# Kernel optimization log

Hardware: AMD Instinct MI355X
Metric: run time of the kernel (lower is better)

## Reference

```python
import jax, jax.numpy as jnp
import numpy as np

BATCH = 4
N_CTX = 1024
D_IN = 512
N_HEADS = 8
D_HEAD = 64
N_VARS = D_IN // D_HEAD  # ConstrainedRead default: n_vars = d_in // d_var = 8
TEMP = 1.0
ATTN_TEMP = float(np.sqrt(D_HEAD))  # attention_temp default = sqrt(d_head)


def setup_inputs() -> dict:
    key = jax.random.key(0)
    k1, k2, k3, k4, k5 = jax.random.split(key, 5)
    x = jax.random.uniform(k1, (BATCH, N_CTX, D_IN), dtype=jnp.float32)
    # causal tril mask, broadcast to batch (matches registered tril buffer usage)
    mask = jnp.broadcast_to(jnp.tril(jnp.ones((N_CTX, N_CTX), dtype=bool)), (BATCH, N_CTX, N_CTX))
    inv_sv = 1.0 / np.sqrt(N_VARS)
    W_K_W = jax.random.normal(k2, (N_HEADS, N_VARS), dtype=jnp.float32) * inv_sv
    W_Q_W = jax.random.normal(k3, (N_HEADS, N_VARS), dtype=jnp.float32) * inv_sv
    W_V_W = jax.random.normal(k4, (N_HEADS, N_VARS), dtype=jnp.float32) * inv_sv
    W_pred_W = jax.random.normal(k5, (N_HEADS, D_HEAD, D_HEAD), dtype=jnp.float32) / np.sqrt(D_HEAD)
    return {"x": x, "mask": mask, "W_K_W": W_K_W, "W_Q_W": W_Q_W, "W_V_W": W_V_W, "W_pred_W": W_pred_W}


def _constrained_read(W):
    # softmax over variables, then block-diagonal-style selector: (h, d_head, d_in)
    probs = jax.nn.softmax(W / TEMP, axis=-1)                 # (h, n_vars)
    eye = jnp.eye(D_HEAD, dtype=probs.dtype)                  # (c, c)
    rm = probs[:, :, None, None] * eye                        # (h, v, c, c)
    # einops 'a b c d -> a d (b c)'
    return jnp.transpose(rm, (0, 3, 1, 2)).reshape(N_HEADS, D_HEAD, D_IN)


def _fixed_bias_table():
    M = N_CTX  # table layout: [-2, linspace(0,-M,M-1)/M, linspace(-M,0,M)/M], shared over heads
    return jnp.concatenate([
        jnp.array([-2.0], dtype=jnp.float32),
        (jnp.linspace(0.0, -float(M), M - 1) / M).astype(jnp.float32),
        (jnp.linspace(-float(M), 0.0, M) / M).astype(jnp.float32),
    ])  # (2M,)


def reference(x, mask, W_K_W, W_Q_W, W_V_W, W_pred_W):
    WK = _constrained_read(W_K_W)
    WQm = _constrained_read(W_Q_W)
    WV = _constrained_read(W_V_W)
    # WPred: out[h,f,d] = sum_e W_Q[h,e,d] * softmax(W)[h,e,f]
    Wp = jax.nn.softmax(W_pred_W / TEMP, axis=-1)
    WQ = jnp.einsum('hed,hef->hfd', WQm, Wp)

    k = jnp.einsum('ihd,bpd->biph', WK, x)   # (b,h,p,dh)
    q = jnp.einsum('ihd,bpd->biph', WQ, x)
    v = jnp.einsum('ihd,bpd->biph', WV, x)

    pre = jnp.einsum('biph,biqh->biqp', k, q)            # (b,h,q,p)
    m = mask[:, None]                                    # (b,1,q,p)
    srow = jnp.where(m, pre, 0.0).sum(-1)                # (b,h,q)
    max_score = srow / (srow + 1e-10)
    pre = pre.at[:, :, :, 0].add(jax.nn.relu(1.0 - max_score))

    nq, nk = pre.shape[-2], pre.shape[-1]
    # relative position gather; %(2M) reproduces torch negative-index wraparound
    rel = (jnp.arange(nk)[None, :] - jnp.arange(nq)[:, None]) % (2 * N_CTX)
    bias = _fixed_bias_table()[rel]                      # (nq,nk), identical per head

    # one_hot_input=True: log(scores + 1e-20) + bias
    pos = jnp.log(pre + 1e-20) + bias[None, None]
    masked = jnp.where(m, pos, -1e30)
    attn = jax.nn.softmax(masked / ATTN_TEMP / TEMP, axis=-1)

    z = jnp.einsum('biph,biqp->biqh', v, attn)           # (b,h,q,dh)
    # einops 'b i q h -> b q (i h)'
    return jnp.transpose(z, (0, 2, 1, 3)).reshape(x.shape[0], nq, N_HEADS * D_HEAD)
```

## Files before the change

### kernel.cpp

```cpp
#include <hip/hip_runtime.h>
#include <math.h>

#define NCTX 1024
#define DIN 512
#define NH 8
#define DH 64

typedef float f32x16 __attribute__((ext_vector_type(16)));
typedef short bf16x8 __attribute__((ext_vector_type(8)));
typedef int i32x4 __attribute__((ext_vector_type(4)));

#define QF_OFF 0
#define KF_OFF (4u * 1024u * 1024u)
#define VF_OFF (8u * 1024u * 1024u)
#define V0_OFF (12u * 1024u * 1024u)

__device__ __forceinline__ bf16x8 asbf(i32x4 v) {
  union { i32x4 i; bf16x8 h; } u;
  u.i = v;
  return u.h;
}

__device__ __forceinline__ bf16x8 mk8(unsigned a, unsigned b, unsigned c,
                                      unsigned d) {
  union { unsigned u[4]; bf16x8 h; } x;
  x.u[0] = a; x.u[1] = b; x.u[2] = c; x.u[3] = d;
  return x.h;
}

__device__ __forceinline__ unsigned cvtpk(float lo, float hi_) {
  unsigned r;
  asm("v_cvt_pk_bf16_f32 %0, %1, %2" : "=v"(r) : "v"(lo), "v"(hi_));
  return r;
}

__device__ __forceinline__ void softmax8(const float* __restrict__ w,
                                         float* __restrict__ p) {
  float mx = w[0];
#pragma unroll
  for (int v = 1; v < 8; ++v) mx = fmaxf(mx, w[v]);
  float s = 0.f;
#pragma unroll
  for (int v = 0; v < 8; ++v) { p[v] = expf(w[v] - mx); s += p[v]; }
  const float inv = 1.f / s;
#pragma unroll
  for (int v = 0; v < 8; ++v) p[v] *= inv;
}

__global__ __launch_bounds__(256) void prep_kernel(
    const float* __restrict__ x, const float* __restrict__ WKw,
    const float* __restrict__ WQw, const float* __restrict__ WVw,
    const float* __restrict__ Wpred, short* __restrict__ Qf,
    short* __restrict__ Kf, short* __restrict__ Vf, float* __restrict__ V0f) {
  const int t = blockIdx.x, ih = blockIdx.y, b = blockIdx.z;
  const int bi = b * NH + ih;
  const int tid = threadIdx.x;

  __shared__ alignas(16) char smem[5 * 8192];
  char* const Ksb = smem;
  char* const Vtb = smem + 8192;
  char* const Q0b = smem + 16384;
  char* const WpT = smem + 24576;
  char* const Qsb = smem + 32768;

  {
    const int e = tid >> 2, sg = tid & 3;
    const float* wr = Wpred + (size_t)(ih * 64 + e) * 64 + sg * 16;
    float e16[16];
    float mx = -1e30f;
#pragma unroll
    for (int j = 0; j < 16; ++j) { e16[j] = wr[j]; mx = fmaxf(mx, e16[j]); }
    mx = fmaxf(mx, __shfl_xor(mx, 1, 4));
    mx = fmaxf(mx, __shfl_xor(mx, 2, 4));
    float s = 0.f;
#pragma unroll
    for (int j = 0; j < 16; ++j) { e16[j] = __expf(e16[j] - mx); s += e16[j]; }
    s += __shfl_xor(s, 1, 4);
    s += __shfl_xor(s, 2, 4);
    const float inv = 1.f / s;
#pragma unroll
    for (int j = 0; j < 16; ++j) {
      const int f = sg * 16 + j;
      const unsigned pz = cvtpk(e16[j] * inv, e16[j] * inv);
      *(unsigned short*)&WpT[f * 128 + ((2 * e) ^ ((f & 7) << 4))] =
          (unsigned short)pz;
    }
  }

  float pk[8], pq8[8], pv[8];
  {
    float w[8];
#pragma unroll
    for (int v = 0; v < 8; ++v) w[v] = WKw[ih * 8 + v];
    softmax8(w, pk);
#pragma unroll
    for (int v = 0; v < 8; ++v) w[v] = WQw[ih * 8 + v];
    softmax8(w, pq8);
#pragma unroll
    for (int v = 0; v < 8; ++v) w[v] = WVw[ih * 8 + v];
    softmax8(w, pv);
  }

  const int rg = tid >> 4, eg = tid & 15;
  const int r0 = rg * 4, e0 = eg * 4;
  float ka[4][4], qa[4][4], va[4][4];
#pragma unroll
  for (int i2 = 0; i2 < 4; ++i2)
#pragma unroll
    for (int j = 0; j < 4; ++j) { ka[i2][j] = 0.f; qa[i2][j] = 0.f; va[i2][j] = 0.f; }

  const float* xb = x + ((size_t)(b * NCTX + t * 64 + r0)) * DIN + e0;
#pragma unroll
  for (int v = 0; v < 8; ++v) {
#pragma unroll
    for (int i2 = 0; i2 < 4; ++i2) {
      const float4 xv = *(const float4*)(xb + (size_t)i2 * DIN + v * 64);
      ka[i2][0] = fmaf(pk[v], xv.x, ka[i2][0]);
      ka[i2][1] = fmaf(pk[v], xv.y, ka[i2][1]);
      ka[i2][2] = fmaf(pk[v], xv.z, ka[i2][2]);
      ka[i2][3] = fmaf(pk[v], xv.w, ka[i2][3]);
      qa[i2][0] = fmaf(pq8[v], xv.x, qa[i2][0]);
      qa[i2][1] = fmaf(pq8[v], xv.y, qa[i2][1]);
      qa[i2][2] = fmaf(pq8[v], xv.z, qa[i2][2]);
      qa[i2][3] = fmaf(pq8[v], xv.w, qa[i2][3]);
      va[i2][0] = fmaf(pv[v], xv.x, va[i2][0]);
      va[i2][1] = fmaf(pv[v], xv.y, va[i2][1]);
      va[i2][2] = fmaf(pv[v], xv.z, va[i2][2]);
      va[i2][3] = fmaf(pv[v], xv.w, va[i2][3]);
    }
  }

  if (t == 0 && rg == 0) {
    *(float4*)(V0f + bi * 64 + e0) =
        make_float4(va[0][0], va[0][1], va[0][2], va[0][3]);
  }

#pragma unroll
  for (int i2 = 0; i2 < 4; ++i2) {
    const int r = r0 + i2;
    const int boff = (2 * e0) ^ ((r & 7) << 4);
    *(uint2*)&Ksb[r * 128 + boff] =
        make_uint2(cvtpk(ka[i2][0], ka[i2][1]), cvtpk(ka[i2][2], ka[i2][3]));
    *(uint2*)&Q0b[r * 128 + boff] =
        make_uint2(cvtpk(qa[i2][0], qa[i2][1]), cvtpk(qa[i2][2], qa[i2][3]));
  }
#pragma unroll
  for (int j = 0; j < 4; ++j) {
    const int rr = e0 + j;
    *(uint2*)&Vtb[rr * 128 + ((2 * r0) ^ ((rr & 7) << 4))] =
        make_uint2(cvtpk(va[0][j], va[1][j]), cvtpk(va[2][j], va[3][j]));
  }
  __syncthreads();

  const int wv = tid >> 6;
  const int l = tid & 63;
  const int lm = l & 31;
  const int hi = l >> 5;

  const size_t fbase = (size_t)bi * 8192 + (size_t)t * 512;
#pragma unroll
  for (int c = 0; c < 2; ++c) {
    const int idx = c * 256 + tid;
    const int pq = idx >> 8, j = (idx >> 6) & 3, ll = idx & 63;
    const int krow = 32 * pq + (ll & 31);
    const i32x4 kfr = *(const i32x4*)
        &Ksb[krow * 128 + ((32 * j + 16 * (ll >> 5)) ^ ((krow & 7) << 4))];
    ((i32x4*)Kf)[fbase + idx] = kfr;
    const int vrow = 32 * (j & 1) + (ll & 31);
    const i32x4 vfr = *(const i32x4*)
        &Vtb[vrow * 128 +
             ((64 * pq + 32 * (j >> 1) + 16 * (ll >> 5)) ^ ((vrow & 7) << 4))];
    ((i32x4*)Vf)[fbase + idx] = vfr;
  }

  {
    const int qq = wv & 1, ff = wv >> 1;
    f32x16 dreg;
#pragma unroll
    for (int r = 0; r < 16; ++r) dreg[r] = 0.f;
    const int arow = 32 * qq + lm;
    const int brow = 32 * ff + lm;
#pragma unroll
    for (int kk = 0; kk < 4; ++kk) {
      const i32x4 af = *(const i32x4*)
          &Q0b[arow * 128 + ((32 * kk + 16 * hi) ^ ((arow & 7) << 4))];
      const i32x4 bfr = *(const i32x4*)
          &WpT[brow * 128 + ((32 * kk + 16 * hi) ^ ((brow & 7) << 4))];
      dreg = __builtin_amdgcn_mfma_f32_32x32x16_bf16(asbf(af), asbf(bfr),
                                                     dreg, 0, 0, 0);
    }
#pragma unroll
    for (int r = 0; r < 16; ++r) {
      const int q = 32 * qq + (r & 3) + 8 * (r >> 2) + 4 * hi;
      const int f = 32 * ff + lm;
      const unsigned pz = cvtpk(dreg[r], dreg[r]);
      *(unsigned short*)&Qsb[q * 128 + ((2 * f) ^ ((q & 7) << 4))] =
          (unsigned short)pz;
    }
  }
  __syncthreads();

#pragma unroll
  for (int c = 0; c < 2; ++c) {
    const int idx = c * 256 + tid;
    const int qq2 = idx >> 8, kk = (idx >> 6) & 3, ll = idx & 63;
    const int row = 32 * qq2 + (ll & 31);
    const i32x4 qfr = *(const i32x4*)
        &Qsb[row * 128 + ((32 * kk + 16 * (ll >> 5)) ^ ((row & 7) << 4))];
    ((i32x4*)Qf)[fbase + idx] = qfr;
  }
}

#if __has_builtin(__builtin_amdgcn_exp2f) && __has_builtin(__builtin_amdgcn_logf)
#define T_LOG(x) __builtin_amdgcn_logf(x)
#define T_EXP(x) __builtin_amdgcn_exp2f(x)
#define T_L 1.7628215e-4f
#define T_DIAG (-0.36067376f)
#else
#define T_LOG(x) __logf(x)
#define T_EXP(x) __expf(x)
#define T_L 1.2219941e-4f
#define T_DIAG (-0.25f)
#endif

__global__ __launch_bounds__(256) void attn_kernel(
    const short* __restrict__ Qf, const short* __restrict__ Kf,
    const short* __restrict__ Vf, float* __restrict__ out) {
  const int bx = blockIdx.x;
  const int a = bx >> 5;
  const int bi = bx & 31;
  const int qt = (a < 16) ? (15 - (a >> 1)) : ((a - 16) >> 1);
  const int qq = a & 1;
  const int b = bi >> 3, ih = bi & 7;
  const int tid = threadIdx.x;
  const int wv = tid >> 6;
  const int pq = wv & 1;
  const int ph = wv >> 1;
  const int l = tid & 63;
  const int hi = l >> 5;
  const int lm = l & 31;

  __shared__ float nbuf[3][32][64];
  __shared__ float rdn[4][32];
  __shared__ float rinv[32];

  const i32x4* Qp = (const i32x4*)Qf + (size_t)bi * 8192 + (size_t)qt * 512 +
                    qq * 256;
  const i32x4* Kp = (const i32x4*)Kf + (size_t)bi * 8192 + pq * 256;
  const i32x4* Vp = (const i32x4*)Vf + (size_t)bi * 8192 + pq * 256;

  bf16x8 qfr[4];
#pragma unroll
  for (int kk = 0; kk < 4; ++kk) qfr[kk] = asbf(Qp[kk * 64 + l]);

  f32x16 num0, num1, st;
#pragma unroll
  for (int r = 0; r < 16; ++r) { num0[r] = 0.f; num1[r] = 0.f; }
  float den = 0.f;
  const int qg = qt * 64 + 32 * qq + lm;
  const int qpb = qg - 32 * pq - 4 * hi;

  i32x4 kK[4], vV[4];

#define LOADK(PT)                                                       \
  do {                                                                  \
    const size_t o_ = (size_t)(PT) * 512;                               \
    _Pragma("unroll") for (int kk = 0; kk < 4; ++kk)                    \
        kK[kk] = Kp[o_ + kk * 64 + l];                                  \
  } while (0)

#define LOADV(PT)                                                       \
  do {                                                                  \
    const size_t o_ = (size_t)(PT) * 512;                               \
    _Pragma("unroll") for (int j = 0; j < 4; ++j)                       \
        vV[j] = Vp[o_ + j * 64 + l];                                    \
  } while (0)

#define QKSTEP()                                                             \
  do {                                                                       \
    _Pragma("unroll") for (int r = 0; r < 16; ++r) st[r] = 0.f;              \
    __builtin_amdgcn_s_setprio(1);                                           \
    _Pragma("unroll") for (int kk = 0; kk < 4; ++kk) st =                    \
        __builtin_amdgcn_mfma_f32_32x32x16_bf16(asbf(kK[kk]), qfr[kk],       \
                                                st, 0, 0, 0);                \
    __builtin_amdgcn_s_setprio(0);                                           \
  } while (0)

#define REPACK_PV()                                                          \
  do {                                                                       \
    asm("v_permlane32_swap_b32 %0, %1" : "+v"(P0), "+v"(P2));                \
    asm("v_permlane32_swap_b32 %0, %1" : "+v"(P1), "+v"(P3));                \
    asm("v_permlane32_swap_b32 %0, %1" : "+v"(P4), "+v"(P6));                \
    asm("v_permlane32_swap_b32 %0, %1" : "+v"(P5), "+v"(P7));                \
    const bf16x8 wf0 = mk8(P0, P1, P2, P3);                                  \
    const bf16x8 wf1 = mk8(P4, P5, P6, P7);                                  \
    __builtin_amdgcn_s_setprio(1);                                           \
    num0 = __builtin_amdgcn_mfma_f32_32x32x16_bf16(wf0, asbf(vV[0]),         \
                                                   num0, 0, 0, 0);           \
    num1 = __builtin_amdgcn_mfma_f32_32x32x16_bf16(wf0, asbf(vV[1]),         \
                                                   num1, 0, 0, 0);           \
    num0 = __builtin_amdgcn_mfma_f32_32x32x16_bf16(wf1, asbf(vV[2]),         \
                                                   num0, 0, 0, 0);           \
    num1 = __builtin_amdgcn_mfma_f32_32x32x16_bf16(wf1, asbf(vV[3]),         \
                                                   num1, 0, 0, 0);           \
    __builtin_amdgcn_s_setprio(0);                                           \
  } while (0)

  if (ph <= qt) {
    LOADK(ph);
    LOADV(ph);
    QKSTEP();
    if (ph + 2 <= qt) LOADK(ph + 2);

#pragma unroll 1
    for (int t = ph; t <= qt; t += 2) {
      const int D0 = qpb - 64 * t;
      const float B0 = (1.0f - (float)D0) * T_L;
      float d4_[4] = {0.f, 0.f, 0.f, 0.f};
      if (t == qt) {
#pragma unroll
        for (int r = 0; r < 16; ++r) {
          const int ro = (r & 3) + 8 * (r >> 2);
          const float pre = st[r];
          float b2 = B0 + (float)ro * T_L;
          b2 = (D0 == ro) ? T_DIAG : b2;
          b2 = (D0 < ro) ? -1e38f : b2;
          st[r] = T_EXP(fmaf(0.125f, T_LOG(pre + 1e-20f), b2));
          d4_[r & 3] += st[r];
        }
      } else {
#pragma unroll
        for (int r = 0; r < 16; ++r) {
          const int ro = (r & 3) + 8 * (r >> 2);
          const float b2 = B0 + (float)ro * T_L;
          st[r] = T_EXP(fmaf(0.125f, T_LOG(st[r] + 1e-20f), b2));
          d4_[r & 3] += st[r];
        }
      }
      den += (d4_[0] + d4_[1]) + (d4_[2] + d4_[3]);
      unsigned P0 = cvtpk(st[0], st[1]), P1 = cvtpk(st[2], st[3]);
      unsigned P2 = cvtpk(st[4], st[5]), P3 = cvtpk(st[6], st[7]);
      unsigned P4 = cvtpk(st[8], st[9]), P5 = cvtpk(st[10], st[11]);
      unsigned P6 = cvtpk(st[12], st[13]), P7 = cvtpk(st[14], st[15]);
      if (t + 2 <= qt) {
        QKSTEP();
        if (t + 4 <= qt) LOADK(t + 4);
      }
      REPACK_PV();
      if (t + 2 <= qt) LOADV(t + 2);
    }
  }

  const float den2 = den + __shfl_xor(den, 32, 64);
  if (hi == 0) rdn[wv][lm] = den2;
  if (wv != 0) {
#pragma unroll
    for (int r = 0; r < 16; ++r) {
      const int row = (r & 3) + 8 * (r >> 2) + 4 * hi;
      nbuf[wv - 1][row][lm] = num0[r];
      nbuf[wv - 1][row][32 + lm] = num1[r];
    }
  }
  __syncthreads();
  if (wv == 0 && hi == 0) {
    rinv[lm] = 1.f / (rdn[0][lm] + rdn[1][lm] + rdn[2][lm] + rdn[3][lm]);
  }
  __syncthreads();
  if (wv == 0) {
#pragma unroll
    for (int r = 0; r < 16; ++r) {
      const int row = (r & 3) + 8 * (r >> 2) + 4 * hi;
      const int qgq = qt * 64 + qq * 32 + row;
      const float iv = rinv[row];
      const float o0 = (num0[r] + nbuf[0][row][lm] + nbuf[1][row][lm] +
                        nbuf[2][row][lm]) * iv;
      const float o1 = (num1[r] + nbuf[0][row][32 + lm] +
                        nbuf[1][row][32 + lm] + nbuf[2][row][32 + lm]) * iv;
      float* op = out + ((size_t)b * NCTX + qgq) * DIN + ih * DH;
      op[lm] = o0;
      op[32 + lm] = o1;
    }
  }
#undef LOADK
#undef LOADV
#undef QKSTEP
#undef REPACK_PV
}

extern "C" void kernel_launch(void* const* d_in, const int* in_sizes, int n_in,
                              void* d_out, int out_size, void* d_ws,
                              size_t ws_size, hipStream_t stream) {
  const float* x = (const float*)d_in[0];
  const float* WKw = (const float*)d_in[2];
  const float* WQw = (const float*)d_in[3];
  const float* WVw = (const float*)d_in[4];
  const float* Wpred = (const float*)d_in[5];
  float* out = (float*)d_out;

  short* Qf = (short*)((char*)d_ws + QF_OFF);
  short* Kf = (short*)((char*)d_ws + KF_OFF);
  short* Vf = (short*)((char*)d_ws + VF_OFF);
  float* V0f = (float*)((char*)d_ws + V0_OFF);

  dim3 block(256);
  dim3 grid1(16, NH, 4);
  hipLaunchKernelGGL(prep_kernel, grid1, block, 0, stream, x, WKw, WQw, WVw,
                     Wpred, Qf, Kf, Vf, V0f);
  dim3 block2(256);
  dim3 grid2(1024);
  hipLaunchKernelGGL(attn_kernel, grid2, block2, 0, stream, Qf, Kf, Vf, out);
}
```

Baseline: 34.67 us.

## Share K/V tiles across two query halves via LDS double buffering

```diff
diff --git a/kernel.cpp b/kernel.cpp
--- a/kernel.cpp
+++ b/kernel.cpp
@@ -32,6 +32,12 @@
   unsigned r;
   asm("v_cvt_pk_bf16_f32 %0, %1, %2" : "=v"(r) : "v"(lo), "v"(hi_));
   return r;
+}
+
+__device__ __forceinline__ void gload_lds16(const i32x4* g, i32x4* lds) {
+  __builtin_amdgcn_global_load_lds(
+      (const __attribute__((address_space(1))) void*)g,
+      (__attribute__((address_space(3))) void*)lds, 16, 0, 0);
 }
 
 __device__ __forceinline__ void softmax8(const float* __restrict__ w,
@@ -229,25 +235,25 @@
   const int bx = blockIdx.x;
   const int a = bx >> 5;
   const int bi = bx & 31;
-  const int qt = (a < 16) ? (15 - (a >> 1)) : ((a - 16) >> 1);
-  const int qq = a & 1;
+  const int qt = (a < 8) ? (15 - a) : (a - 8);
   const int b = bi >> 3, ih = bi & 7;
   const int tid = threadIdx.x;
   const int wv = tid >> 6;
-  const int pq = wv & 1;
-  const int ph = wv >> 1;
   const int l = tid & 63;
   const int hi = l >> 5;
   const int lm = l & 31;
-
-  __shared__ float nbuf[3][32][64];
-  __shared__ float rdn[4][32];
-  __shared__ float rinv[32];
+  const int pq = wv & 1;
+  const int qq = wv >> 1;
+
+  __shared__ i32x4 kvbuf[2][1024];
+  __shared__ float num_l[2][32][64];
+  __shared__ float rdn[2][2][32];
+  __shared__ float rinv[2][32];
 
   const i32x4* Qp = (const i32x4*)Qf + (size_t)bi * 8192 + (size_t)qt * 512 +
                     qq * 256;
-  const i32x4* Kp = (const i32x4*)Kf + (size_t)bi * 8192 + pq * 256;
-  const i32x4* Vp = (const i32x4*)Vf + (size_t)bi * 8192 + pq * 256;
+  const i32x4* Kg = (const i32x4*)Kf + (size_t)bi * 8192;
+  const i32x4* Vg = (const i32x4*)Vf + (size_t)bi * 8192;
 
   bf16x8 qfr[4];
 #pragma unroll
@@ -260,131 +266,117 @@
   const int qg = qt * 64 + 32 * qq + lm;
   const int qpb = qg - 32 * pq - 4 * hi;
 
-  i32x4 kK[4], vV[4];
-
-#define LOADK(PT)                                                       \
-  do {                                                                  \
-    const size_t o_ = (size_t)(PT) * 512;                               \
-    _Pragma("unroll") for (int kk = 0; kk < 4; ++kk)                    \
-        kK[kk] = Kp[o_ + kk * 64 + l];                                  \
+#define STAGE(T, BUF)                                                        \
+  do {                                                                       \
+    const size_t o_ = (size_t)(T) * 512;                                     \
+    _Pragma("unroll") for (int c = 0; c < 4; ++c) {                          \
+      const int grp = wv * 4 + c;                                            \
+      const int idx = grp * 64 + l;                                          \
+      const i32x4* src = (grp < 8) ? (Kg + o_ + idx) : (Vg + o_ + idx - 512);\
+      gload_lds16(src, &kvbuf[BUF][grp * 64]);                               \
+    }                                                                        \
   } while (0)
 
-#define LOADV(PT)                                                       \
-  do {                                                                  \
-    const size_t o_ = (size_t)(PT) * 512;                               \
-    _Pragma("unroll") for (int j = 0; j < 4; ++j)                       \
-        vV[j] = Vp[o_ + j * 64 + l];                                    \
-  } while (0)
-
-#define QKSTEP()                                                             \
-  do {                                                                       \
-    _Pragma("unroll") for (int r = 0; r < 16; ++r) st[r] = 0.f;              \
-    __builtin_amdgcn_s_setprio(1);                                           \
-    _Pragma("unroll") for (int kk = 0; kk < 4; ++kk) st =                    \
-        __builtin_amdgcn_mfma_f32_32x32x16_bf16(asbf(kK[kk]), qfr[kk],       \
-                                                st, 0, 0, 0);                \
-    __builtin_amdgcn_s_setprio(0);                                           \
-  } while (0)
-
-#define REPACK_PV()                                                          \
-  do {                                                                       \
-    asm("v_permlane32_swap_b32 %0, %1" : "+v"(P0), "+v"(P2));                \
-    asm("v_permlane32_swap_b32 %0, %1" : "+v"(P1), "+v"(P3));                \
-    asm("v_permlane32_swap_b32 %0, %1" : "+v"(P4), "+v"(P6));                \
-    asm("v_permlane32_swap_b32 %0, %1" : "+v"(P5), "+v"(P7));                \
-    const bf16x8 wf0 = mk8(P0, P1, P2, P3);                                  \
-    const bf16x8 wf1 = mk8(P4, P5, P6, P7);                                  \
-    __builtin_amdgcn_s_setprio(1);                                           \
-    num0 = __builtin_amdgcn_mfma_f32_32x32x16_bf16(wf0, asbf(vV[0]),         \
-                                                   num0, 0, 0, 0);           \
-    num1 = __builtin_amdgcn_mfma_f32_32x32x16_bf16(wf0, asbf(vV[1]),         \
-                                                   num1, 0, 0, 0);           \
-    num0 = __builtin_amdgcn_mfma_f32_32x32x16_bf16(wf1, asbf(vV[2]),         \
-                                                   num0, 0, 0, 0);           \
-    num1 = __builtin_amdgcn_mfma_f32_32x32x16_bf16(wf1, asbf(vV[3]),         \
-                                                   num1, 0, 0, 0);           \
-    __builtin_amdgcn_s_setprio(0);                                           \
-  } while (0)
-
-  if (ph <= qt) {
-    LOADK(ph);
-    LOADV(ph);
-    QKSTEP();
-    if (ph + 2 <= qt) LOADK(ph + 2);
+  STAGE(0, 0);
+  __syncthreads();
 
 #pragma unroll 1
-    for (int t = ph; t <= qt; t += 2) {
-      const int D0 = qpb - 64 * t;
-      const float B0 = (1.0f - (float)D0) * T_L;
-      float d4_[4] = {0.f, 0.f, 0.f, 0.f};
-      if (t == qt) {
-#pragma unroll
-        for (int r = 0; r < 16; ++r) {
-          const int ro = (r & 3) + 8 * (r >> 2);
-          const float pre = st[r];
-          float b2 = B0 + (float)ro * T_L;
-          b2 = (D0 == ro) ? T_DIAG : b2;
-          b2 = (D0 < ro) ? -1e38f : b2;
-          st[r] = T_EXP(fmaf(0.125f, T_LOG(pre + 1e-20f), b2));
-          d4_[r & 3] += st[r];
-        }
-      } else {
-#pragma unroll
-        for (int r = 0; r < 16; ++r) {
-          const int ro = (r & 3) + 8 * (r >> 2);
-          const float b2 = B0 + (float)ro * T_L;
-          st[r] = T_EXP(fmaf(0.125f, T_LOG(st[r] + 1e-20f), b2));
-          d4_[r & 3] += st[r];
-        }
+  for (int t = 0; t <= qt; ++t) {
+    const int cur = t & 1;
+    if (t + 1 <= qt) STAGE(t + 1, cur ^ 1);
+
+    const i32x4 kK0 = kvbuf[cur][pq * 256 + l];
+    const i32x4 kK1 = kvbuf[cur][pq * 256 + 64 + l];
+    const i32x4 kK2 = kvbuf[cur][pq * 256 + 128 + l];
+    const i32x4 kK3 = kvbuf[cur][pq * 256 + 192 + l];
+#pragma unroll
+    for (int r = 0; r < 16; ++r) st[r] = 0.f;
+    __builtin_amdgcn_s_setprio(1);
+    st = __builtin_amdgcn_mfma_f32_32x32x16_bf16(asbf(kK0), qfr[0], st, 0, 0, 0);
+    st = __builtin_amdgcn_mfma_f32_32x32x16_bf16(asbf(kK1), qfr[1], st, 0, 0, 0);
+    st = __builtin_amdgcn_mfma_f32_32x32x16_bf16(asbf(kK2), qfr[2], st, 0, 0, 0);
+    st = __builtin_amdgcn_mfma_f32_32x32x16_bf16(asbf(kK3), qfr[3], st, 0, 0, 0);
+    __builtin_amdgcn_s_setprio(0);
+
+    const int D0 = qpb - 64 * t;
+    const float B0 = (1.0f - (float)D0) * T_L;
+    float d4_[4] = {0.f, 0.f, 0.f, 0.f};
+    if (t == qt) {
+#pragma unroll
+      for (int r = 0; r < 16; ++r) {
+        const int ro = (r & 3) + 8 * (r >> 2);
+        const float pre = st[r];
+        float b2 = B0 + (float)ro * T_L;
+        b2 = (D0 == ro) ? T_DIAG : b2;
+        b2 = (D0 < ro) ? -1e38f : b2;
+        st[r] = T_EXP(fmaf(0.125f, T_LOG(pre + 1e-20f), b2));
+        d4_[r & 3] += st[r];
       }
-      den += (d4_[0] + d4_[1]) + (d4_[2] + d4_[3]);
-      unsigned P0 = cvtpk(st[0], st[1]), P1 = cvtpk(st[2], st[3]);
-      unsigned P2 = cvtpk(st[4], st[5]), P3 = cvtpk(st[6], st[7]);
-      unsigned P4 = cvtpk(st[8], st[9]), P5 = cvtpk(st[10], st[11]);
-      unsigned P6 = cvtpk(st[12], st[13]), P7 = cvtpk(st[14], st[15]);
-      if (t + 2 <= qt) {
-        QKSTEP();
-        if (t + 4 <= qt) LOADK(t + 4);
+    } else {
+#pragma unroll
+      for (int r = 0; r < 16; ++r) {
+        const int ro = (r & 3) + 8 * (r >> 2);
+        const float b2 = B0 + (float)ro * T_L;
+        st[r] = T_EXP(fmaf(0.125f, T_LOG(st[r] + 1e-20f), b2));
+        d4_[r & 3] += st[r];
       }
-      REPACK_PV();
-      if (t + 2 <= qt) LOADV(t + 2);
-    }
+    }
+    den += (d4_[0] + d4_[1]) + (d4_[2] + d4_[3]);
+
+    unsigned P0 = cvtpk(st[0], st[1]), P1 = cvtpk(st[2], st[3]);
+    unsigned P2 = cvtpk(st[4], st[5]), P3 = cvtpk(st[6], st[7]);
+    unsigned P4 = cvtpk(st[8], st[9]), P5 = cvtpk(st[10], st[11]);
+    unsigned P6 = cvtpk(st[12], st[13]), P7 = cvtpk(st[14], st[15]);
+    asm("v_permlane32_swap_b32 %0, %1" : "+v"(P0), "+v"(P2));
+    asm("v_permlane32_swap_b32 %0, %1" : "+v"(P1), "+v"(P3));
+    asm("v_permlane32_swap_b32 %0, %1" : "+v"(P4), "+v"(P6));
+    asm("v_permlane32_swap_b32 %0, %1" : "+v"(P5), "+v"(P7));
+    const bf16x8 wf0 = mk8(P0, P1, P2, P3);
+    const bf16x8 wf1 = mk8(P4, P5, P6, P7);
+
+    const i32x4 vV0 = kvbuf[cur][512 + pq * 256 + l];
+    const i32x4 vV1 = kvbuf[cur][512 + pq * 256 + 64 + l];
+    const i32x4 vV2 = kvbuf[cur][512 + pq * 256 + 128 + l];
+    const i32x4 vV3 = kvbuf[cur][512 + pq * 256 + 192 + l];
+    __builtin_amdgcn_s_setprio(1);
+    num0 = __builtin_amdgcn_mfma_f32_32x32x16_bf16(wf0, asbf(vV0), num0, 0, 0, 0);
+    num1 = __builtin_amdgcn_mfma_f32_32x32x16_bf16(wf0, asbf(vV1), num1, 0, 0, 0);
+    num0 = __builtin_amdgcn_mfma_f32_32x32x16_bf16(wf1, asbf(vV2), num0, 0, 0, 0);
+    num1 = __builtin_amdgcn_mfma_f32_32x32x16_bf16(wf1, asbf(vV3), num1, 0, 0, 0);
+    __builtin_amdgcn_s_setprio(0);
+
+    __syncthreads();
   }
 
   const float den2 = den + __shfl_xor(den, 32, 64);
-  if (hi == 0) rdn[wv][lm] = den2;
-  if (wv != 0) {
+  if (hi == 0) rdn[qq][pq][lm] = den2;
+  if (pq == 1) {
 #pragma unroll
     for (int r = 0; r < 16; ++r) {
       const int row = (r & 3) + 8 * (r >> 2) + 4 * hi;
-      nbuf[wv - 1][row][lm] = num0[r];
-      nbuf[wv - 1][row][32 + lm] = num1[r];
+      num_l[qq][row][lm] = num0[r];
+      num_l[qq][row][32 + lm] = num1[r];
     }
   }
   __syncthreads();
-  if (wv == 0 && hi == 0) {
-    rinv[lm] = 1.f / (rdn[0][lm] + rdn[1][lm] + rdn[2][lm] + rdn[3][lm]);
+  if (pq == 1 && hi == 0) {
+    rinv[qq][lm] = 1.f / (rdn[qq][0][lm] + rdn[qq][1][lm]);
   }
   __syncthreads();
-  if (wv == 0) {
+  if (pq == 0) {
 #pragma unroll
     for (int r = 0; r < 16; ++r) {
       const int row = (r & 3) + 8 * (r >> 2) + 4 * hi;
       const int qgq = qt * 64 + qq * 32 + row;
-      const float iv = rinv[row];
-      const float o0 = (num0[r] + nbuf[0][row][lm] + nbuf[1][row][lm] +
-                        nbuf[2][row][lm]) * iv;
-      const float o1 = (num1[r] + nbuf[0][row][32 + lm] +
-                        nbuf[1][row][32 + lm] + nbuf[2][row][32 + lm]) * iv;
+      const float iv = rinv[qq][row];
+      const float o0 = (num0[r] + num_l[qq][row][lm]) * iv;
+      const float o1 = (num1[r] + num_l[qq][row][32 + lm]) * iv;
       float* op = out + ((size_t)b * NCTX + qgq) * DIN + ih * DH;
       op[lm] = o0;
       op[32 + lm] = o1;
     }
   }
-#undef LOADK
-#undef LOADV
-#undef QKSTEP
-#undef REPACK_PV
+#undef STAGE
 }
 
 extern "C" void kernel_launch(void* const* d_in, const int* in_sizes, int n_in,
@@ -407,6 +399,6 @@
   hipLaunchKernelGGL(prep_kernel, grid1, block, 0, stream, x, WKw, WQw, WVw,
                      Wpred, Qf, Kf, Vf, V0f);
   dim3 block2(256);
-  dim3 grid2(1024);
+  dim3 grid2(512);
   hipLaunchKernelGGL(attn_kernel, grid2, block2, 0, stream, Qf, Kf, Vf, out);
 }
```

Result: no change. 34.92 us (+0.7%).
